# Optimization experiments

Hardware: AMD Instinct MI355X
Metric: run time of the kernel (lower is better)

Reference implementation:

```python
import jax, jax.numpy as jnp
import numpy as np
import math

B, H, S, D = 2, 16, 2048, 64


def setup_inputs() -> dict:
    key = jax.random.key(0)
    kq, kk, kv = jax.random.split(key, 3)
    q = jax.random.normal(kq, (B, H, S, D), dtype=jnp.float32)
    k = jax.random.normal(kk, (B, H, S, D), dtype=jnp.float32)
    v = jax.random.normal(kv, (B, H, S, D), dtype=jnp.float32)
    # causal lower-triangular mask, broadcastable to [B, H, S, S]
    mask = jnp.tril(jnp.ones((S, S), dtype=jnp.int32))[None, None, :, :]
    return {"q": q, "k": k, "v": v, "mask": mask}


def reference(q, k, v, mask):
    d_tensor = q.shape[-1]
    # scores: [B, H, S, S] = q @ k^T / sqrt(d)
    scores = jnp.einsum("bhqd,bhkd->bhqk", q, k) / math.sqrt(d_tensor)
    scores = jnp.where(mask == 0, jnp.float32(-100000.0), scores)
    attn = jax.nn.softmax(scores, axis=-1)
    out = jnp.einsum("bhqk,bhkd->bhqd", attn, v)
    return (out, attn)
```

## Files before the change

kernel.cpp:

```cpp
#include <hip/hip_runtime.h>

#define S_LEN 2048
#define D_DIM 64
#define NBH   32
#define BQ    128
#define SCALE2 0.1803368801f
#define KST   72

typedef _Float16 half8  __attribute__((ext_vector_type(8)));
typedef _Float16 half4  __attribute__((ext_vector_type(4)));
typedef _Float16 half2v __attribute__((ext_vector_type(2)));
typedef float    fx4    __attribute__((ext_vector_type(4)));

#define BAR() do {                                            \
    asm volatile("s_waitcnt lgkmcnt(0)" ::: "memory");        \
    __builtin_amdgcn_s_barrier();                             \
    asm volatile("" ::: "memory");                            \
} while (0)

__global__ __launch_bounds__(512, 4)
void attn_fused(const float* __restrict__ Q, const float* __restrict__ K,
                const float* __restrict__ V, float* __restrict__ Out,
                float* __restrict__ Attn) {
    const int bh  = blockIdx.x;
    const int qt  = (int)(gridDim.y - 1) - (int)blockIdx.y;
    const int q0  = qt * BQ;
    const int T   = 2 * qt + 2;

    const int tid  = threadIdx.x;
    const int lane = tid & 63;
    const int w    = tid >> 6;
    const int ln15 = lane & 15;
    const int quad = lane >> 4;

    __shared__ _Float16 smem[6 * 64 * KST];
    _Float16 (*kb0)[KST] = (_Float16 (*)[KST])&smem[0];
    _Float16 (*kb1)[KST] = (_Float16 (*)[KST])&smem[64 * KST];
    _Float16 (*vb0)[KST] = (_Float16 (*)[KST])&smem[2 * 64 * KST];
    _Float16 (*vb1)[KST] = (_Float16 (*)[KST])&smem[3 * 64 * KST];
    _Float16 (*pw)[KST]  = (_Float16 (*)[KST])&smem[4 * 64 * KST + w * 16 * KST];
    _Float16 (*q_s)[KST] = kb0;

    const float* Qb = Q + ((size_t)bh * S_LEN + q0) * D_DIM;
    const float* Kb = K + (size_t)bh * S_LEN * D_DIM;
    const float* Vb = V + (size_t)bh * S_LEN * D_DIM;

    const int sr  = tid >> 4;
    const int sc4 = tid & 15;
    const int vp2 = tid & 31;
    const int vc  = tid >> 5;

    const float4* ks0 = (const float4*)Kb;
    float4 kf0 = ks0[tid], kf1 = ks0[512 + tid];
    {
        const float4* src = (const float4*)Qb;
        #pragma unroll
        for (int u = 0; u < 4; ++u) {
            int i = u * 512 + tid;
            int r = i >> 4, c4 = i & 15;
            float4 f = src[i];
            half4 h = {(_Float16)(f.x * SCALE2), (_Float16)(f.y * SCALE2),
                       (_Float16)(f.z * SCALE2), (_Float16)(f.w * SCALE2)};
            *(half4*)&q_s[r][c4 * 4] = h;
        }
    }
    BAR();

    const int mrow = w * 16 + ln15;
    const half8 a_q0 = *(const half8*)&q_s[mrow][quad * 8];
    const half8 a_q1 = *(const half8*)&q_s[mrow][32 + quad * 8];
    BAR();

    const int wrow0 = q0 + w * 16;
    const int qrow0 = wrow0 + quad * 4;

    float l_r[4] = {0.f, 0.f, 0.f, 0.f};

    for (int t = 0; t < T; ++t) {
        _Float16 (*kb)[KST] = (t & 1) ? kb1 : kb0;
        {
            half4 h0 = {(_Float16)kf0.x, (_Float16)kf0.y, (_Float16)kf0.z, (_Float16)kf0.w};
            half4 h1 = {(_Float16)kf1.x, (_Float16)kf1.y, (_Float16)kf1.z, (_Float16)kf1.w};
            *(half4*)&kb[sr +  0][sc4 * 4] = h0;
            *(half4*)&kb[sr + 32][sc4 * 4] = h1;
        }
        BAR();

        if (t + 1 < T) {
            const float4* kn = (const float4*)(Kb + (size_t)(t + 1) * 64 * D_DIM);
            kf0 = kn[tid]; kf1 = kn[512 + tid];
        }

        const int j0 = t * 64;
        if (j0 > wrow0 + 15) continue;

        fx4 sC[4];
        #pragma unroll
        for (int nt = 0; nt < 4; ++nt) {
            fx4 z = {0.f, 0.f, 0.f, 0.f};
            half8 b0 = *(const half8*)&kb[nt * 16 + ln15][quad * 8];
            half8 b1 = *(const half8*)&kb[nt * 16 + ln15][32 + quad * 8];
            z = __builtin_amdgcn_mfma_f32_16x16x32_f16(a_q0, b0, z, 0, 0, 0);
            z = __builtin_amdgcn_mfma_f32_16x16x32_f16(a_q1, b1, z, 0, 0, 0);
            sC[nt] = z;
        }

        if (j0 + 63 <= wrow0) {
            #pragma unroll
            for (int nt = 0; nt < 4; ++nt)
                #pragma unroll
                for (int r = 0; r < 4; ++r)
                    l_r[r] += exp2f(sC[nt][r]);
        } else {
            #pragma unroll
            for (int nt = 0; nt < 4; ++nt) {
                int jc = j0 + nt * 16 + ln15;
                #pragma unroll
                for (int r = 0; r < 4; ++r) {
                    float x = (jc <= qrow0 + r) ? sC[nt][r] : -1e30f;
                    l_r[r] += exp2f(x);
                }
            }
        }
    }
    BAR();

    float inv_l[4];
    #pragma unroll
    for (int r = 0; r < 4; ++r) {
        float s = l_r[r];
        s += __shfl_xor(s, 1);
        s += __shfl_xor(s, 2);
        s += __shfl_xor(s, 4);
        s += __shfl_xor(s, 8);
        inv_l[r] = 1.0f / s;
    }

    fx4 oacc[4];
    #pragma unroll
    for (int dt = 0; dt < 4; ++dt) oacc[dt] = (fx4){0.f, 0.f, 0.f, 0.f};

    float4 vf0, vf1;
    {
        kf0 = ks0[tid]; kf1 = ks0[512 + tid];
        const float4* vs = (const float4*)Vb;
        vf0 = vs[(2 * vp2 + 0) * 16 + vc];
        vf1 = vs[(2 * vp2 + 1) * 16 + vc];
    }

    for (int t = 0; t < T; ++t) {
        const int j0 = t * 64;
        _Float16 (*kb)[KST] = (t & 1) ? kb1 : kb0;
        _Float16 (*vb)[KST] = (t & 1) ? vb1 : vb0;

        {
            half4 h0 = {(_Float16)kf0.x, (_Float16)kf0.y, (_Float16)kf0.z, (_Float16)kf0.w};
            half4 h1 = {(_Float16)kf1.x, (_Float16)kf1.y, (_Float16)kf1.z, (_Float16)kf1.w};
            *(half4*)&kb[sr +  0][sc4 * 4] = h0;
            *(half4*)&kb[sr + 32][sc4 * 4] = h1;
            #pragma unroll
            for (int i = 0; i < 4; ++i) {
                half2v h = {(_Float16)vf0[i], (_Float16)vf1[i]};
                *(half2v*)&vb[vc * 4 + i][2 * vp2] = h;
            }
        }
        BAR();

        if (t + 1 < T) {
            const float4* kn = (const float4*)(Kb + (size_t)(t + 1) * 64 * D_DIM);
            kf0 = kn[tid]; kf1 = kn[512 + tid];
            const float4* vn = (const float4*)(Vb + (size_t)(t + 1) * 64 * D_DIM);
            vf0 = vn[(2 * vp2 + 0) * 16 + vc];
            vf1 = vn[(2 * vp2 + 1) * 16 + vc];
        }

        if (j0 > wrow0 + 15) {
            #pragma unroll
            for (int nt = 0; nt < 4; ++nt) {
                int jc = j0 + nt * 16 + ln15;
                #pragma unroll
                for (int r = 0; r < 4; ++r)
                    Attn[((size_t)bh * S_LEN + (size_t)(qrow0 + r)) * S_LEN + jc] = 0.0f;
            }
            continue;
        }

        fx4 sC[4];
        #pragma unroll
        for (int nt = 0; nt < 4; ++nt) {
            fx4 z = {0.f, 0.f, 0.f, 0.f};
            half8 b0 = *(const half8*)&kb[nt * 16 + ln15][quad * 8];
            half8 b1 = *(const half8*)&kb[nt * 16 + ln15][32 + quad * 8];
            z = __builtin_amdgcn_mfma_f32_16x16x32_f16(a_q0, b0, z, 0, 0, 0);
            z = __builtin_amdgcn_mfma_f32_16x16x32_f16(a_q1, b1, z, 0, 0, 0);
            sC[nt] = z;
        }

        if (j0 + 63 <= wrow0) {
            #pragma unroll
            for (int nt = 0; nt < 4; ++nt) {
                int jc = j0 + nt * 16 + ln15;
                #pragma unroll
                for (int r = 0; r < 4; ++r) {
                    float p = exp2f(sC[nt][r]) * inv_l[r];
                    Attn[((size_t)bh * S_LEN + (size_t)(qrow0 + r)) * S_LEN + jc] = p;
                    pw[quad * 4 + r][nt * 16 + ln15] = (_Float16)p;
                }
            }
        } else {
            #pragma unroll
            for (int nt = 0; nt < 4; ++nt) {
                int jc = j0 + nt * 16 + ln15;
                #pragma unroll
                for (int r = 0; r < 4; ++r) {
                    float x = (jc <= qrow0 + r) ? sC[nt][r] : -1e30f;
                    float p = exp2f(x) * inv_l[r];
                    Attn[((size_t)bh * S_LEN + (size_t)(qrow0 + r)) * S_LEN + jc] = p;
                    pw[quad * 4 + r][nt * 16 + ln15] = (_Float16)p;
                }
            }
        }

        {
            half8 a_p0 = *(const half8*)&pw[ln15][quad * 8];
            half8 a_p1 = *(const half8*)&pw[ln15][32 + quad * 8];
            #pragma unroll
            for (int dt = 0; dt < 4; ++dt) {
                half8 bv0 = *(const half8*)&vb[dt * 16 + ln15][quad * 8];
                half8 bv1 = *(const half8*)&vb[dt * 16 + ln15][32 + quad * 8];
                oacc[dt] = __builtin_amdgcn_mfma_f32_16x16x32_f16(a_p0, bv0, oacc[dt], 0, 0, 0);
                oacc[dt] = __builtin_amdgcn_mfma_f32_16x16x32_f16(a_p1, bv1, oacc[dt], 0, 0, 0);
            }
        }
    }

    #pragma unroll
    for (int dt = 0; dt < 4; ++dt) {
        #pragma unroll
        for (int r = 0; r < 4; ++r) {
            size_t oidx = ((size_t)bh * S_LEN + (size_t)(qrow0 + r)) * D_DIM + dt * 16 + ln15;
            Out[oidx] = oacc[dt][r];
        }
    }

    {
        const int jend = q0 + BQ;
        const int rowlen4 = (S_LEN - jend) >> 2;
        if (rowlen4 > 0) {
            fx4 z = {0.f, 0.f, 0.f, 0.f};
            for (int r = w; r < BQ; r += 8) {
                fx4* dst = (fx4*)(Attn + ((size_t)bh * S_LEN + (size_t)(q0 + r)) * S_LEN + jend);
                for (int c = lane; c < rowlen4; c += 64) dst[c] = z;
            }
        }
    }
}

extern "C" void kernel_launch(void* const* d_in, const int* in_sizes, int n_in,
                              void* d_out, int out_size, void* d_ws, size_t ws_size,
                              hipStream_t stream) {
    const float* q = (const float*)d_in[0];
    const float* k = (const float*)d_in[1];
    const float* v = (const float*)d_in[2];
    float* out  = (float*)d_out;
    float* attn = out + (size_t)NBH * S_LEN * D_DIM;
    dim3 grid(NBH, S_LEN / BQ);
    attn_fused<<<grid, 512, 0, stream>>>(q, k, v, out, attn);
}
```

Measured before the change: 643.1 us.

## Precompute fp16 K and transposed V in workspace before the fused attention kernel

Adds a prep kernel that converts K to fp16 and V to fp16 stored transposed per 64-key tile, writing both into the workspace. The main kernel then loads half8 vectors straight into shared memory, with no per-tile float-to-half conversion or scattered transpose stores. This halves the K/V read bytes in the attention kernel and removes redundant conversions repeated across query tiles. The cost is an extra launch and a full read/write pass over K and V. An fp32 fallback kernel is kept for when the workspace is too small.

```diff
diff --git a/kernel.cpp b/kernel.cpp
--- a/kernel.cpp
+++ b/kernel.cpp
@@ -6,6 +6,7 @@
 #define BQ    128
 #define SCALE2 0.1803368801f
 #define KST   72
+#define KVH_ELEMS ((size_t)NBH * S_LEN * D_DIM)
 
 typedef _Float16 half8  __attribute__((ext_vector_type(8)));
 typedef _Float16 half4  __attribute__((ext_vector_type(4)));
@@ -18,9 +19,51 @@
     asm volatile("" ::: "memory");                            \
 } while (0)
 
+__global__ __launch_bounds__(256)
+void prep_kv(const float* __restrict__ K, const float* __restrict__ V,
+             _Float16* __restrict__ Kh, _Float16* __restrict__ Vt) {
+    const int bh  = blockIdx.x;
+    const int j0  = blockIdx.y * 256;
+    const int tid = threadIdx.x;
+
+    const float4* ks = (const float4*)(K + ((size_t)bh * S_LEN + j0) * D_DIM);
+    _Float16* kd = Kh + ((size_t)bh * S_LEN + j0) * D_DIM;
+    #pragma unroll
+    for (int u = 0; u < 16; ++u) {
+        int i = u * 256 + tid;
+        float4 f = ks[i];
+        half4 h = {(_Float16)f.x, (_Float16)f.y, (_Float16)f.z, (_Float16)f.w};
+        *(half4*)&kd[i * 4] = h;
+    }
+
+    const float4* vs = (const float4*)(V + ((size_t)bh * S_LEN + j0) * D_DIM);
+    const int c4 = tid & 15;
+    const int jq = tid >> 4;
+    #pragma unroll
+    for (int u = 0; u < 4; ++u) {
+        int q  = u * 16 + jq;
+        int jb = q * 4;
+        float4 g0 = vs[(jb + 0) * 16 + c4];
+        float4 g1 = vs[(jb + 1) * 16 + c4];
+        float4 g2 = vs[(jb + 2) * 16 + c4];
+        float4 g3 = vs[(jb + 3) * 16 + c4];
+        int t   = (j0 + jb) >> 6;
+        int jin = (j0 + jb) & 63;
+        _Float16* vd = Vt + (size_t)bh * (S_LEN * D_DIM) + (size_t)t * 4096 + jin;
+        half4 h0 = {(_Float16)g0.x, (_Float16)g1.x, (_Float16)g2.x, (_Float16)g3.x};
+        half4 h1 = {(_Float16)g0.y, (_Float16)g1.y, (_Float16)g2.y, (_Float16)g3.y};
+        half4 h2 = {(_Float16)g0.z, (_Float16)g1.z, (_Float16)g2.z, (_Float16)g3.z};
+        half4 h3 = {(_Float16)g0.w, (_Float16)g1.w, (_Float16)g2.w, (_Float16)g3.w};
+        *(half4*)&vd[(c4 * 4 + 0) * 64] = h0;
+        *(half4*)&vd[(c4 * 4 + 1) * 64] = h1;
+        *(half4*)&vd[(c4 * 4 + 2) * 64] = h2;
+        *(half4*)&vd[(c4 * 4 + 3) * 64] = h3;
+    }
+}
+
 __global__ __launch_bounds__(512, 4)
-void attn_fused(const float* __restrict__ Q, const float* __restrict__ K,
-                const float* __restrict__ V, float* __restrict__ Out,
+void attn_fused(const float* __restrict__ Q, const _Float16* __restrict__ Kh,
+                const _Float16* __restrict__ Vt, float* __restrict__ Out,
                 float* __restrict__ Attn) {
     const int bh  = blockIdx.x;
     const int qt  = (int)(gridDim.y - 1) - (int)blockIdx.y;
@@ -41,17 +84,14 @@
     _Float16 (*pw)[KST]  = (_Float16 (*)[KST])&smem[4 * 64 * KST + w * 16 * KST];
     _Float16 (*q_s)[KST] = kb0;
 
-    const float* Qb = Q + ((size_t)bh * S_LEN + q0) * D_DIM;
-    const float* Kb = K + (size_t)bh * S_LEN * D_DIM;
-    const float* Vb = V + (size_t)bh * S_LEN * D_DIM;
-
-    const int sr  = tid >> 4;
-    const int sc4 = tid & 15;
-    const int vp2 = tid & 31;
-    const int vc  = tid >> 5;
-
-    const float4* ks0 = (const float4*)Kb;
-    float4 kf0 = ks0[tid], kf1 = ks0[512 + tid];
+    const float*    Qb  = Q  + ((size_t)bh * S_LEN + q0) * D_DIM;
+    const _Float16* Khb = Kh + (size_t)bh * S_LEN * D_DIM;
+    const _Float16* Vtb = Vt + (size_t)bh * S_LEN * D_DIM;
+
+    const int sr2 = tid >> 3;
+    const int cu  = tid & 7;
+
+    half8 kh = *(const half8*)(Khb + (size_t)tid * 8);
     {
         const float4* src = (const float4*)Qb;
         #pragma unroll
@@ -78,18 +118,11 @@
 
     for (int t = 0; t < T; ++t) {
         _Float16 (*kb)[KST] = (t & 1) ? kb1 : kb0;
-        {
-            half4 h0 = {(_Float16)kf0.x, (_Float16)kf0.y, (_Float16)kf0.z, (_Float16)kf0.w};
-            half4 h1 = {(_Float16)kf1.x, (_Float16)kf1.y, (_Float16)kf1.z, (_Float16)kf1.w};
-            *(half4*)&kb[sr +  0][sc4 * 4] = h0;
-            *(half4*)&kb[sr + 32][sc4 * 4] = h1;
-        }
+        *(half8*)&kb[sr2][cu * 8] = kh;
         BAR();
 
-        if (t + 1 < T) {
-            const float4* kn = (const float4*)(Kb + (size_t)(t + 1) * 64 * D_DIM);
-            kf0 = kn[tid]; kf1 = kn[512 + tid];
-        }
+        if (t + 1 < T)
+            kh = *(const half8*)(Khb + (size_t)(t + 1) * 4096 + (size_t)tid * 8);
 
         const int j0 = t * 64;
         if (j0 > wrow0 + 15) continue;
@@ -140,38 +173,21 @@
     #pragma unroll
     for (int dt = 0; dt < 4; ++dt) oacc[dt] = (fx4){0.f, 0.f, 0.f, 0.f};
 
-    float4 vf0, vf1;
-    {
-        kf0 = ks0[tid]; kf1 = ks0[512 + tid];
-        const float4* vs = (const float4*)Vb;
-        vf0 = vs[(2 * vp2 + 0) * 16 + vc];
-        vf1 = vs[(2 * vp2 + 1) * 16 + vc];
-    }
+    kh = *(const half8*)(Khb + (size_t)tid * 8);
+    half8 vh = *(const half8*)(Vtb + (size_t)tid * 8);
 
     for (int t = 0; t < T; ++t) {
         const int j0 = t * 64;
         _Float16 (*kb)[KST] = (t & 1) ? kb1 : kb0;
         _Float16 (*vb)[KST] = (t & 1) ? vb1 : vb0;
 
-        {
-            half4 h0 = {(_Float16)kf0.x, (_Float16)kf0.y, (_Float16)kf0.z, (_Float16)kf0.w};
-            half4 h1 = {(_Float16)kf1.x, (_Float16)kf1.y, (_Float16)kf1.z, (_Float16)kf1.w};
-            *(half4*)&kb[sr +  0][sc4 * 4] = h0;
-            *(half4*)&kb[sr + 32][sc4 * 4] = h1;
-            #pragma unroll
-            for (int i = 0; i < 4; ++i) {
-                half2v h = {(_Float16)vf0[i], (_Float16)vf1[i]};
-                *(half2v*)&vb[vc * 4 + i][2 * vp2] = h;
-            }
-        }
+        *(half8*)&kb[sr2][cu * 8] = kh;
+        *(half8*)&vb[sr2][cu * 8] = vh;
         BAR();
 
         if (t + 1 < T) {
-            const float4* kn = (const float4*)(Kb + (size_t)(t + 1) * 64 * D_DIM);
-            kf0 = kn[tid]; kf1 = kn[512 + tid];
-            const float4* vn = (const float4*)(Vb + (size_t)(t + 1) * 64 * D_DIM);
-            vf0 = vn[(2 * vp2 + 0) * 16 + vc];
-            vf1 = vn[(2 * vp2 + 1) * 16 + vc];
+            kh = *(const half8*)(Khb + (size_t)(t + 1) * 4096 + (size_t)tid * 8);
+            vh = *(const half8*)(Vtb + (size_t)(t + 1) * 4096 + (size_t)tid * 8);
         }
 
         if (j0 > wrow0 + 15) {
@@ -243,6 +259,216 @@
         }
     }
 
+    {
+        const int jend = q0 + BQ;
+        const int rowlen4 = (S_LEN - jend) >> 2;
+        if (rowlen4 > 0) {
+            fx4 z = {0.f, 0.f, 0.f, 0.f};
+            for (int r = w; r < BQ; r += 8) {
+                fx4* dst = (fx4*)(Attn + ((size_t)bh * S_LEN + (size_t)(q0 + r)) * S_LEN + jend);
+                for (int c = lane; c < rowlen4; c += 64) dst[c] = z;
+            }
+        }
+    }
+}
+
+__global__ __launch_bounds__(512, 4)
+void attn_fused_f32(const float* __restrict__ Q, const float* __restrict__ K,
+                    const float* __restrict__ V, float* __restrict__ Out,
+                    float* __restrict__ Attn) {
+    const int bh  = blockIdx.x;
+    const int qt  = (int)(gridDim.y - 1) - (int)blockIdx.y;
+    const int q0  = qt * BQ;
+    const int T   = 2 * qt + 2;
+    const int tid  = threadIdx.x;
+    const int lane = tid & 63;
+    const int w    = tid >> 6;
+    const int ln15 = lane & 15;
+    const int quad = lane >> 4;
+    __shared__ _Float16 smem[6 * 64 * KST];
+    _Float16 (*kb0)[KST] = (_Float16 (*)[KST])&smem[0];
+    _Float16 (*kb1)[KST] = (_Float16 (*)[KST])&smem[64 * KST];
+    _Float16 (*vb0)[KST] = (_Float16 (*)[KST])&smem[2 * 64 * KST];
+    _Float16 (*vb1)[KST] = (_Float16 (*)[KST])&smem[3 * 64 * KST];
+    _Float16 (*pw)[KST]  = (_Float16 (*)[KST])&smem[4 * 64 * KST + w * 16 * KST];
+    _Float16 (*q_s)[KST] = kb0;
+    const float* Qb = Q + ((size_t)bh * S_LEN + q0) * D_DIM;
+    const float* Kb = K + (size_t)bh * S_LEN * D_DIM;
+    const float* Vb = V + (size_t)bh * S_LEN * D_DIM;
+    const int sr  = tid >> 4;
+    const int sc4 = tid & 15;
+    const int vp2 = tid & 31;
+    const int vc  = tid >> 5;
+    const float4* ks0 = (const float4*)Kb;
+    float4 kf0 = ks0[tid], kf1 = ks0[512 + tid];
+    {
+        const float4* src = (const float4*)Qb;
+        #pragma unroll
+        for (int u = 0; u < 4; ++u) {
+            int i = u * 512 + tid;
+            int r = i >> 4, c4 = i & 15;
+            float4 f = src[i];
+            half4 h = {(_Float16)(f.x * SCALE2), (_Float16)(f.y * SCALE2),
+                       (_Float16)(f.z * SCALE2), (_Float16)(f.w * SCALE2)};
+            *(half4*)&q_s[r][c4 * 4] = h;
+        }
+    }
+    BAR();
+    const int mrow = w * 16 + ln15;
+    const half8 a_q0 = *(const half8*)&q_s[mrow][quad * 8];
+    const half8 a_q1 = *(const half8*)&q_s[mrow][32 + quad * 8];
+    BAR();
+    const int wrow0 = q0 + w * 16;
+    const int qrow0 = wrow0 + quad * 4;
+    float l_r[4] = {0.f, 0.f, 0.f, 0.f};
+    for (int t = 0; t < T; ++t) {
+        _Float16 (*kb)[KST] = (t & 1) ? kb1 : kb0;
+        {
+            half4 h0 = {(_Float16)kf0.x, (_Float16)kf0.y, (_Float16)kf0.z, (_Float16)kf0.w};
+            half4 h1 = {(_Float16)kf1.x, (_Float16)kf1.y, (_Float16)kf1.z, (_Float16)kf1.w};
+            *(half4*)&kb[sr +  0][sc4 * 4] = h0;
+            *(half4*)&kb[sr + 32][sc4 * 4] = h1;
+        }
+        BAR();
+        if (t + 1 < T) {
+            const float4* kn = (const float4*)(Kb + (size_t)(t + 1) * 64 * D_DIM);
+            kf0 = kn[tid]; kf1 = kn[512 + tid];
+        }
+        const int j0 = t * 64;
+        if (j0 > wrow0 + 15) continue;
+        fx4 sC[4];
+        #pragma unroll
+        for (int nt = 0; nt < 4; ++nt) {
+            fx4 z = {0.f, 0.f, 0.f, 0.f};
+            half8 b0 = *(const half8*)&kb[nt * 16 + ln15][quad * 8];
+            half8 b1 = *(const half8*)&kb[nt * 16 + ln15][32 + quad * 8];
+            z = __builtin_amdgcn_mfma_f32_16x16x32_f16(a_q0, b0, z, 0, 0, 0);
+            z = __builtin_amdgcn_mfma_f32_16x16x32_f16(a_q1, b1, z, 0, 0, 0);
+            sC[nt] = z;
+        }
+        if (j0 + 63 <= wrow0) {
+            #pragma unroll
+            for (int nt = 0; nt < 4; ++nt)
+                #pragma unroll
+                for (int r = 0; r < 4; ++r) l_r[r] += exp2f(sC[nt][r]);
+        } else {
+            #pragma unroll
+            for (int nt = 0; nt < 4; ++nt) {
+                int jc = j0 + nt * 16 + ln15;
+                #pragma unroll
+                for (int r = 0; r < 4; ++r) {
+                    float x = (jc <= qrow0 + r) ? sC[nt][r] : -1e30f;
+                    l_r[r] += exp2f(x);
+                }
+            }
+        }
+    }
+    BAR();
+    float inv_l[4];
+    #pragma unroll
+    for (int r = 0; r < 4; ++r) {
+        float s = l_r[r];
+        s += __shfl_xor(s, 1); s += __shfl_xor(s, 2);
+        s += __shfl_xor(s, 4); s += __shfl_xor(s, 8);
+        inv_l[r] = 1.0f / s;
+    }
+    fx4 oacc[4];
+    #pragma unroll
+    for (int dt = 0; dt < 4; ++dt) oacc[dt] = (fx4){0.f, 0.f, 0.f, 0.f};
+    float4 vf0, vf1;
+    {
+        kf0 = ks0[tid]; kf1 = ks0[512 + tid];
+        const float4* vs = (const float4*)Vb;
+        vf0 = vs[(2 * vp2 + 0) * 16 + vc];
+        vf1 = vs[(2 * vp2 + 1) * 16 + vc];
+    }
+    for (int t = 0; t < T; ++t) {
+        const int j0 = t * 64;
+        _Float16 (*kb)[KST] = (t & 1) ? kb1 : kb0;
+        _Float16 (*vb)[KST] = (t & 1) ? vb1 : vb0;
+        {
+            half4 h0 = {(_Float16)kf0.x, (_Float16)kf0.y, (_Float16)kf0.z, (_Float16)kf0.w};
+            half4 h1 = {(_Float16)kf1.x, (_Float16)kf1.y, (_Float16)kf1.z, (_Float16)kf1.w};
+            *(half4*)&kb[sr +  0][sc4 * 4] = h0;
+            *(half4*)&kb[sr + 32][sc4 * 4] = h1;
+            #pragma unroll
+            for (int i = 0; i < 4; ++i) {
+                half2v h = {(_Float16)vf0[i], (_Float16)vf1[i]};
+                *(half2v*)&vb[vc * 4 + i][2 * vp2] = h;
+            }
+        }
+        BAR();
+        if (t + 1 < T) {
+            const float4* kn = (const float4*)(Kb + (size_t)(t + 1) * 64 * D_DIM);
+            kf0 = kn[tid]; kf1 = kn[512 + tid];
+            const float4* vn = (const float4*)(Vb + (size_t)(t + 1) * 64 * D_DIM);
+            vf0 = vn[(2 * vp2 + 0) * 16 + vc];
+            vf1 = vn[(2 * vp2 + 1) * 16 + vc];
+        }
+        if (j0 > wrow0 + 15) {
+            #pragma unroll
+            for (int nt = 0; nt < 4; ++nt) {
+                int jc = j0 + nt * 16 + ln15;
+                #pragma unroll
+                for (int r = 0; r < 4; ++r)
+                    Attn[((size_t)bh * S_LEN + (size_t)(qrow0 + r)) * S_LEN + jc] = 0.0f;
+            }
+            continue;
+        }
+        fx4 sC[4];
+        #pragma unroll
+        for (int nt = 0; nt < 4; ++nt) {
+            fx4 z = {0.f, 0.f, 0.f, 0.f};
+            half8 b0 = *(const half8*)&kb[nt * 16 + ln15][quad * 8];
+            half8 b1 = *(const half8*)&kb[nt * 16 + ln15][32 + quad * 8];
+            z = __builtin_amdgcn_mfma_f32_16x16x32_f16(a_q0, b0, z, 0, 0, 0);
+            z = __builtin_amdgcn_mfma_f32_16x16x32_f16(a_q1, b1, z, 0, 0, 0);
+            sC[nt] = z;
+        }
+        if (j0 + 63 <= wrow0) {
+            #pragma unroll
+            for (int nt = 0; nt < 4; ++nt) {
+                int jc = j0 + nt * 16 + ln15;
+                #pragma unroll
+                for (int r = 0; r < 4; ++r) {
+                    float p = exp2f(sC[nt][r]) * inv_l[r];
+                    Attn[((size_t)bh * S_LEN + (size_t)(qrow0 + r)) * S_LEN + jc] = p;
+                    pw[quad * 4 + r][nt * 16 + ln15] = (_Float16)p;
+                }
+            }
+        } else {
+            #pragma unroll
+            for (int nt = 0; nt < 4; ++nt) {
+                int jc = j0 + nt * 16 + ln15;
+                #pragma unroll
+                for (int r = 0; r < 4; ++r) {
+                    float x = (jc <= qrow0 + r) ? sC[nt][r] : -1e30f;
+                    float p = exp2f(x) * inv_l[r];
+                    Attn[((size_t)bh * S_LEN + (size_t)(qrow0 + r)) * S_LEN + jc] = p;
+                    pw[quad * 4 + r][nt * 16 + ln15] = (_Float16)p;
+                }
+            }
+        }
+        {
+            half8 a_p0 = *(const half8*)&pw[ln15][quad * 8];
+            half8 a_p1 = *(const half8*)&pw[ln15][32 + quad * 8];
+            #pragma unroll
+            for (int dt = 0; dt < 4; ++dt) {
+                half8 bv0 = *(const half8*)&vb[dt * 16 + ln15][quad * 8];
+                half8 bv1 = *(const half8*)&vb[dt * 16 + ln15][32 + quad * 8];
+                oacc[dt] = __builtin_amdgcn_mfma_f32_16x16x32_f16(a_p0, bv0, oacc[dt], 0, 0, 0);
+                oacc[dt] = __builtin_amdgcn_mfma_f32_16x16x32_f16(a_p1, bv1, oacc[dt], 0, 0, 0);
+            }
+        }
+    }
+    #pragma unroll
+    for (int dt = 0; dt < 4; ++dt) {
+        #pragma unroll
+        for (int r = 0; r < 4; ++r) {
+            size_t oidx = ((size_t)bh * S_LEN + (size_t)(qrow0 + r)) * D_DIM + dt * 16 + ln15;
+            Out[oidx] = oacc[dt][r];
+        }
+    }
     {
         const int jend = q0 + BQ;
         const int rowlen4 = (S_LEN - jend) >> 2;
@@ -265,5 +491,14 @@
     float* out  = (float*)d_out;
     float* attn = out + (size_t)NBH * S_LEN * D_DIM;
     dim3 grid(NBH, S_LEN / BQ);
-    attn_fused<<<grid, 512, 0, stream>>>(q, k, v, out, attn);
+
+    const size_t need = 2 * KVH_ELEMS * sizeof(_Float16);
+    if (ws_size >= need) {
+        _Float16* Kh = (_Float16*)d_ws;
+        _Float16* Vt = Kh + KVH_ELEMS;
+        prep_kv<<<dim3(NBH, 8), 256, 0, stream>>>(k, v, Kh, Vt);
+        attn_fused<<<grid, 512, 0, stream>>>(q, Kh, Vt, out, attn);
+    } else {
+        attn_fused_f32<<<grid, 512, 0, stream>>>(q, k, v, out, attn);
+    }
 }
```

After: 637.1 us. Within noise of the previous version (-0.9%).
